# Kernel tuning notes

Hardware: AMD Instinct MI355X
Metric: run time of the kernel (lower is better)

Reference implementation:

```python
import jax, jax.numpy as jnp
import numpy as np

B, F_, P, C, H, W = 2048, 1024, 64, 1, 8, 8


def setup_inputs() -> dict:
    key = jax.random.key(0)
    k1, k2 = jax.random.split(key)
    x = jax.random.normal(k1, (B, C, H, W), dtype=jnp.float32)
    # sampled weights ww = sampler(get_features()): (out_dim, n_samples, *inp_shape)
    ww = jax.random.normal(k2, (F_, P, C, H, W), dtype=jnp.float32)
    scale = jnp.ones((1, F_), dtype=jnp.float32)
    bias = jnp.zeros((1, F_), dtype=jnp.float32)
    return {"x": x, "ww": ww, "scale": scale, "bias": bias}


def reference(x, ww, scale, bias):
    # x: (b, C, H, W) -> (b, i);  ww: (f, p, C, H, W) -> (f, p, i)
    xf = x.reshape(x.shape[0], -1)
    wwf = ww.reshape(ww.shape[0], ww.shape[1], -1)
    # scores: (b, p, f) -- the large intermediate a fused kernel would avoid
    scores = jnp.einsum('bi,fpi->bpf', xf, wwf)
    out = jnp.max(scores, axis=1)          # max-pool over samples p -> (b, f)
    out = out * scale + bias               # rescale=True, add_bias=True
    return out                             # act = Identity
```

## Files before the change

kernel.cpp:

```cpp
#include <hip/hip_runtime.h>

typedef __bf16 bf16x8 __attribute__((ext_vector_type(8)));
typedef float f32x16 __attribute__((ext_vector_type(16)));

constexpr int kB = 2048, kF = 1024, kP = 64, kK = 64;
constexpr size_t WWPK_BYTES = (size_t)kF * kP * kK * 2;


__global__ __launch_bounds__(256, 8)
void pack_kernel(const float* __restrict__ x, const float* __restrict__ ww,
                 __bf16* __restrict__ wwpk, __bf16* __restrict__ xpk) {
  const int bx = blockIdx.x, tid = threadIdx.x;
  if (bx < 2048) {
    const int g = bx * 256 + tid;
    const float4 lo = *reinterpret_cast<const float4*>(ww + (size_t)g * 8);
    const float4 hi = *reinterpret_cast<const float4*>(ww + (size_t)g * 8 + 4);
    const int f = g >> 9, rem = g & 511;
    const int p = rem >> 3, k8 = rem & 7;
    const int ks = k8 >> 1, half = k8 & 1, mt = p >> 5, p31 = p & 31;
    const int chunk = ((f * 4 + ks) * 2 + half) * 64 + mt * 32 + p31;
    bf16x8 h;
    h[0] = (__bf16)lo.x; h[1] = (__bf16)lo.y; h[2] = (__bf16)lo.z; h[3] = (__bf16)lo.w;
    h[4] = (__bf16)hi.x; h[5] = (__bf16)hi.y; h[6] = (__bf16)hi.z; h[7] = (__bf16)hi.w;
    *reinterpret_cast<bf16x8*>(wwpk + (size_t)chunk * 8) = h;
  } else {
    const int g = (bx - 2048) * 256 + tid;
    const float4 lo = *reinterpret_cast<const float4*>(x + (size_t)g * 8);
    const float4 hi = *reinterpret_cast<const float4*>(x + (size_t)g * 8 + 4);
    const int b = g >> 3, k8 = g & 7;
    const int bt = b >> 5, b31 = b & 31;
    const int chunk = (bt * 8 + k8) * 32 + b31;
    bf16x8 h;
    h[0] = (__bf16)lo.x; h[1] = (__bf16)lo.y; h[2] = (__bf16)lo.z; h[3] = (__bf16)lo.w;
    h[4] = (__bf16)hi.x; h[5] = (__bf16)hi.y; h[6] = (__bf16)hi.z; h[7] = (__bf16)hi.w;
    *reinterpret_cast<bf16x8*>(xpk + (size_t)chunk * 8) = h;
  }
}

__global__ __launch_bounds__(256, 2)
void affine_max_mfma(const __bf16* __restrict__ wwpk, const __bf16* __restrict__ xpk,
                     const float* __restrict__ scale, const float* __restrict__ bias,
                     float* __restrict__ out) {
  __shared__ float s_out[512 * 10];

  const int tid = threadIdx.x, bx = blockIdx.x;
  const int xcd = bx & 7, j = bx >> 3;
  const int fchunk = xcd * 16 + (j & 15);
  const int bgroup = j >> 4;
  const int f0 = fchunk * 8;
  const int b0 = bgroup * 512;

  const int wv = tid >> 6, lane = tid & 63, l31 = lane & 31, half = lane >> 5;

  const char* wbase = reinterpret_cast<const char*>(wwpk) + half * 1024 + l31 * 16;
  bf16x8 afr[2][2][4];
#pragma unroll
  for (int fi = 0; fi < 2; ++fi) {
    const size_t fb = (size_t)(f0 + wv * 2 + fi) * 8192;
#pragma unroll
    for (int mt = 0; mt < 2; ++mt)
#pragma unroll
      for (int ks = 0; ks < 4; ++ks)
        afr[fi][mt][ks] =
            *reinterpret_cast<const bf16x8*>(wbase + fb + ks * 2048 + mt * 512);
  }

  const char* xbase = reinterpret_cast<const char*>(xpk) +
                      (size_t)(bgroup * 16) * 4096 + half * 512 + l31 * 16;
  auto loadB = [&](int t, bf16x8 (&dst)[4]) {
#pragma unroll
    for (int ks = 0; ks < 4; ++ks)
      dst[ks] = *reinterpret_cast<const bf16x8*>(xbase + t * 4096 + ks * 1024);
  };
  auto compute = [&](int t, bf16x8 (&bfr)[4]) {
    f32x16 acc[2][2] = {};
#pragma unroll
    for (int ks = 0; ks < 4; ++ks)
#pragma unroll
      for (int fi = 0; fi < 2; ++fi)
#pragma unroll
        for (int mt = 0; mt < 2; ++mt)
          acc[fi][mt] = __builtin_amdgcn_mfma_f32_32x32x16_bf16(
              afr[fi][mt][ks], bfr[ks], acc[fi][mt], 0, 0, 0);
#pragma unroll
    for (int fi = 0; fi < 2; ++fi) {
      float a[16];
#pragma unroll
      for (int i = 0; i < 16; ++i) a[i] = fmaxf(acc[fi][0][i], acc[fi][1][i]);
#pragma unroll
      for (int s = 8; s >= 1; s >>= 1)
#pragma unroll
        for (int i = 0; i < s; ++i) a[i] = fmaxf(a[i], a[i + s]);
      const float v = fmaxf(a[0], __shfl_xor(a[0], 32));
      if (lane < 32) s_out[(t * 32 + l31) * 10 + wv * 2 + fi] = v;
    }
  };

  bf16x8 bA[4], bB[4];
  loadB(0, bA);
#pragma unroll 1
  for (int t = 0; t < 14; t += 2) {
    loadB(t + 1, bB);
    compute(t, bA);
    loadB(t + 2, bA);
    compute(t + 1, bB);
  }
  loadB(15, bB);
  compute(14, bA);
  compute(15, bB);

  __syncthreads();

  const int c4 = (tid & 1) * 4;
  const float4 scl = *reinterpret_cast<const float4*>(scale + f0 + c4);
  const float4 bia = *reinterpret_cast<const float4*>(bias + f0 + c4);
#pragma unroll
  for (int i = 0; i < 4; ++i) {
    const int row = i * 128 + (tid >> 1);
    const float2 u0 = *reinterpret_cast<const float2*>(&s_out[row * 10 + c4]);
    const float2 u1 = *reinterpret_cast<const float2*>(&s_out[row * 10 + c4 + 2]);
    float4 r;
    r.x = u0.x * scl.x + bia.x;
    r.y = u0.y * scl.y + bia.y;
    r.z = u1.x * scl.z + bia.z;
    r.w = u1.y * scl.w + bia.w;
    *reinterpret_cast<float4*>(out + (size_t)(b0 + row) * kF + f0 + c4) = r;
  }
}

extern "C" void kernel_launch(void* const* d_in, const int* in_sizes, int n_in,
                              void* d_out, int out_size, void* d_ws, size_t ws_size,
                              hipStream_t stream) {
  const float* x = (const float*)d_in[0];
  const float* ww = (const float*)d_in[1];
  const float* scale = (const float*)d_in[2];
  const float* bias = (const float*)d_in[3];
  float* out = (float*)d_out;
  __bf16* wwpk = (__bf16*)d_ws;
  __bf16* xpk = (__bf16*)((char*)d_ws + WWPK_BYTES);

  hipLaunchKernelGGL(pack_kernel, dim3(2048 + 64), dim3(256), 0, stream,
                     x, ww, wwpk, xpk);
  hipLaunchKernelGGL(affine_max_mfma, dim3(512), dim3(256), 0, stream,
                     wwpk, xpk, scale, bias, out);
}
```

Before: 91.27 us.

## Fuse bf16 packing of x and ww into the MFMA max-pool kernel via LDS

Removes the separate pack kernel and its global workspace round trip. Each block now loads fp32 x and ww tiles directly, converts them to bf16, and writes them into shared memory in MFMA fragment layout. Weight fragments are staged through LDS in four rounds, and results are kept in registers before being written to a reused LDS buffer. This saves a launch and the 8 MB bf16 write/read, but each block re-reads fp32 x (bgroup shared by 128 blocks), and the larger LDS footprint may reduce occupancy.

Result: slower. 97.52 us (+6.8%).

```diff
diff --git a/kernel.cpp b/kernel.cpp
--- a/kernel.cpp
+++ b/kernel.cpp
@@ -4,74 +4,86 @@
 typedef float f32x16 __attribute__((ext_vector_type(16)));
 
 constexpr int kB = 2048, kF = 1024, kP = 64, kK = 64;
-constexpr size_t WWPK_BYTES = (size_t)kF * kP * kK * 2;
-
-
-__global__ __launch_bounds__(256, 8)
-void pack_kernel(const float* __restrict__ x, const float* __restrict__ ww,
-                 __bf16* __restrict__ wwpk, __bf16* __restrict__ xpk) {
-  const int bx = blockIdx.x, tid = threadIdx.x;
-  if (bx < 2048) {
-    const int g = bx * 256 + tid;
-    const float4 lo = *reinterpret_cast<const float4*>(ww + (size_t)g * 8);
-    const float4 hi = *reinterpret_cast<const float4*>(ww + (size_t)g * 8 + 4);
-    const int f = g >> 9, rem = g & 511;
-    const int p = rem >> 3, k8 = rem & 7;
-    const int ks = k8 >> 1, half = k8 & 1, mt = p >> 5, p31 = p & 31;
-    const int chunk = ((f * 4 + ks) * 2 + half) * 64 + mt * 32 + p31;
-    bf16x8 h;
-    h[0] = (__bf16)lo.x; h[1] = (__bf16)lo.y; h[2] = (__bf16)lo.z; h[3] = (__bf16)lo.w;
-    h[4] = (__bf16)hi.x; h[5] = (__bf16)hi.y; h[6] = (__bf16)hi.z; h[7] = (__bf16)hi.w;
-    *reinterpret_cast<bf16x8*>(wwpk + (size_t)chunk * 8) = h;
-  } else {
-    const int g = (bx - 2048) * 256 + tid;
-    const float4 lo = *reinterpret_cast<const float4*>(x + (size_t)g * 8);
-    const float4 hi = *reinterpret_cast<const float4*>(x + (size_t)g * 8 + 4);
-    const int b = g >> 3, k8 = g & 7;
-    const int bt = b >> 5, b31 = b & 31;
-    const int chunk = (bt * 8 + k8) * 32 + b31;
-    bf16x8 h;
-    h[0] = (__bf16)lo.x; h[1] = (__bf16)lo.y; h[2] = (__bf16)lo.z; h[3] = (__bf16)lo.w;
-    h[4] = (__bf16)hi.x; h[5] = (__bf16)hi.y; h[6] = (__bf16)hi.z; h[7] = (__bf16)hi.w;
-    *reinterpret_cast<bf16x8*>(xpk + (size_t)chunk * 8) = h;
-  }
-}
 
 __global__ __launch_bounds__(256, 2)
-void affine_max_mfma(const __bf16* __restrict__ wwpk, const __bf16* __restrict__ xpk,
-                     const float* __restrict__ scale, const float* __restrict__ bias,
-                     float* __restrict__ out) {
-  __shared__ float s_out[512 * 10];
+void affine_max_fused(const float* __restrict__ x, const float* __restrict__ ww,
+                      const float* __restrict__ scale, const float* __restrict__ bias,
+                      float* __restrict__ out) {
+  __shared__ __align__(16) char s_x[64 * 1024];
+  __shared__ __align__(16) char s_ww[16 * 1024];
 
   const int tid = threadIdx.x, bx = blockIdx.x;
-  const int xcd = bx & 7, j = bx >> 3;
-  const int fchunk = xcd * 16 + (j & 15);
-  const int bgroup = j >> 4;
+  const int fchunk = (bx & 7) * 16 + ((bx >> 3) & 15);
+  const int bgroup = bx >> 7;
   const int f0 = fchunk * 8;
   const int b0 = bgroup * 512;
 
   const int wv = tid >> 6, lane = tid & 63, l31 = lane & 31, half = lane >> 5;
 
-  const char* wbase = reinterpret_cast<const char*>(wwpk) + half * 1024 + l31 * 16;
-  bf16x8 afr[2][2][4];
 #pragma unroll
-  for (int fi = 0; fi < 2; ++fi) {
-    const size_t fb = (size_t)(f0 + wv * 2 + fi) * 8192;
+  for (int it = 0; it < 4; ++it) {
+    const int g = it * 256 + tid;
+    const int r = g >> 1, h = g & 1;
+    const float* src = x + ((size_t)(b0 + r) * kK + h * 32);
+    float4 v[8];
 #pragma unroll
-    for (int mt = 0; mt < 2; ++mt)
+    for (int j = 0; j < 8; ++j) v[j] = reinterpret_cast<const float4*>(src)[j];
+    const int bt = r >> 5, b31 = r & 31;
 #pragma unroll
-      for (int ks = 0; ks < 4; ++ks)
-        afr[fi][mt][ks] =
-            *reinterpret_cast<const bf16x8*>(wbase + fb + ks * 2048 + mt * 512);
+    for (int q = 0; q < 2; ++q)
+#pragma unroll
+      for (int hf = 0; hf < 2; ++hf) {
+        const float4 a = v[q * 4 + hf * 2], b = v[q * 4 + hf * 2 + 1];
+        bf16x8 hh;
+        hh[0] = (__bf16)a.x; hh[1] = (__bf16)a.y; hh[2] = (__bf16)a.z; hh[3] = (__bf16)a.w;
+        hh[4] = (__bf16)b.x; hh[5] = (__bf16)b.y; hh[6] = (__bf16)b.z; hh[7] = (__bf16)b.w;
+        *reinterpret_cast<bf16x8*>(s_x + bt * 4096 + (h * 2 + q) * 1024 +
+                                   hf * 512 + b31 * 16) = hh;
+      }
   }
 
-  const char* xbase = reinterpret_cast<const char*>(xpk) +
-                      (size_t)(bgroup * 16) * 4096 + half * 512 + l31 * 16;
+  bf16x8 afr[2][2][4];
+#pragma unroll 1
+  for (int rd = 0; rd < 4; ++rd) {
+    const int fl2 = tid >> 7, rem = tid & 127, p = rem >> 1, h = rem & 1;
+    const float* src = ww + ((size_t)(f0 + rd * 2 + fl2) * (kP * kK) + p * kK + h * 32);
+    float4 v[8];
+#pragma unroll
+    for (int j = 0; j < 8; ++j) v[j] = reinterpret_cast<const float4*>(src)[j];
+    __syncthreads();
+    const int mt = p >> 5, p31 = p & 31;
+#pragma unroll
+    for (int q = 0; q < 2; ++q)
+#pragma unroll
+      for (int hf = 0; hf < 2; ++hf) {
+        const float4 a = v[q * 4 + hf * 2], b = v[q * 4 + hf * 2 + 1];
+        bf16x8 hh;
+        hh[0] = (__bf16)a.x; hh[1] = (__bf16)a.y; hh[2] = (__bf16)a.z; hh[3] = (__bf16)a.w;
+        hh[4] = (__bf16)b.x; hh[5] = (__bf16)b.y; hh[6] = (__bf16)b.z; hh[7] = (__bf16)b.w;
+        *reinterpret_cast<bf16x8*>(s_ww + fl2 * 8192 + (h * 2 + q) * 2048 +
+                                   hf * 1024 + mt * 512 + p31 * 16) = hh;
+      }
+    __syncthreads();
+    if (wv == rd) {
+#pragma unroll
+      for (int fi = 0; fi < 2; ++fi)
+#pragma unroll
+        for (int m2 = 0; m2 < 2; ++m2)
+#pragma unroll
+          for (int ks = 0; ks < 4; ++ks)
+            afr[fi][m2][ks] = *reinterpret_cast<const bf16x8*>(
+                s_ww + fi * 8192 + ks * 2048 + half * 1024 + m2 * 512 + l31 * 16);
+    }
+  }
+  __syncthreads();
+
+  const char* xb = s_x + half * 512 + l31 * 16;
   auto loadB = [&](int t, bf16x8 (&dst)[4]) {
 #pragma unroll
     for (int ks = 0; ks < 4; ++ks)
-      dst[ks] = *reinterpret_cast<const bf16x8*>(xbase + t * 4096 + ks * 1024);
+      dst[ks] = *reinterpret_cast<const bf16x8*>(xb + t * 4096 + ks * 1024);
   };
+  float vres[16][2];
   auto compute = [&](int t, bf16x8 (&bfr)[4]) {
     f32x16 acc[2][2] = {};
 #pragma unroll
@@ -91,8 +103,7 @@
       for (int s = 8; s >= 1; s >>= 1)
 #pragma unroll
         for (int i = 0; i < s; ++i) a[i] = fmaxf(a[i], a[i + s]);
-      const float v = fmaxf(a[0], __shfl_xor(a[0], 32));
-      if (lane < 32) s_out[(t * 32 + l31) * 10 + wv * 2 + fi] = v;
+      vres[t][fi] = fmaxf(a[0], __shfl_xor(a[0], 32));
     }
   };
 
@@ -109,6 +120,15 @@
   compute(14, bA);
   compute(15, bB);
 
+  __syncthreads();
+
+  float* s_out = reinterpret_cast<float*>(s_x);
+  if (lane < 32) {
+#pragma unroll
+    for (int t = 0; t < 16; ++t)
+      *reinterpret_cast<float2*>(s_out + (size_t)(t * 32 + l31) * 10 + wv * 2) =
+          float2{vres[t][0], vres[t][1]};
+  }
   __syncthreads();
 
   const int c4 = (tid & 1) * 4;
@@ -136,11 +156,6 @@
   const float* scale = (const float*)d_in[2];
   const float* bias = (const float*)d_in[3];
   float* out = (float*)d_out;
-  __bf16* wwpk = (__bf16*)d_ws;
-  __bf16* xpk = (__bf16*)((char*)d_ws + WWPK_BYTES);
-
-  hipLaunchKernelGGL(pack_kernel, dim3(2048 + 64), dim3(256), 0, stream,
-                     x, ww, wwpk, xpk);
-  hipLaunchKernelGGL(affine_max_mfma, dim3(512), dim3(256), 0, stream,
-                     wwpk, xpk, scale, bias, out);
+  hipLaunchKernelGGL(affine_max_fused, dim3(512), dim3(256), 0, stream,
+                     x, ww, scale, bias, out);
 }
```
